# Kernel optimization log

Hardware: AMD Instinct MI355X
Metric: run time of the kernel (lower is better)

Reference implementation:

```python
import jax, jax.numpy as jnp
import numpy as np
from jax.ops import segment_sum

N_NODES = 100000
N_EDGES = 3200000
NUM_FEATURES = 256


def setup_inputs() -> dict:
    key = jax.random.key(0)
    ks = jax.random.split(key, 12)
    def lin(k, fan_in, fan_out):
        bound = 1.0 / np.sqrt(fan_in)
        kw, kb = jax.random.split(k)
        W = jax.random.uniform(kw, (fan_in, fan_out), jnp.float32, -bound, bound)
        b = jax.random.uniform(kb, (fan_out,), jnp.float32, -bound, bound)
        return W, b
    x = jax.random.normal(ks[0], (N_NODES, NUM_FEATURES), jnp.float32)
    edge_index = jax.random.randint(ks[1], (2, N_EDGES), 0, N_NODES, jnp.int64 if jax.config.jax_enable_x64 else jnp.int32)
    W1, b1 = lin(ks[2], NUM_FEATURES, 64)
    W2, b2 = lin(ks[3], 64, 32)
    W3, b3 = lin(ks[4], 32, 16)
    Ws02, bs02 = lin(ks[5], NUM_FEATURES, 32)
    Ws03, bs03 = lin(ks[6], NUM_FEATURES, 16)
    Ws13, bs13 = lin(ks[7], 64, 16)
    Wout, bout = lin(ks[8], 16, 1)
    return dict(x=x, edge_index=edge_index, W1=W1, b1=b1, W2=W2, b2=b2,
                W3=W3, b3=b3, Ws02=Ws02, bs02=bs02, Ws03=Ws03, bs03=bs03,
                Ws13=Ws13, bs13=bs13, Wout=Wout, bout=bout)


def _deg_inv_sqrt(edge_index, n_nodes):
    # gcn_norm with self-loops: degree counted at target nodes, +1 for self-loop
    dst = edge_index[1]
    deg = segment_sum(jnp.ones(edge_index.shape[1], jnp.float32), dst, num_segments=n_nodes) + 1.0
    return jnp.where(deg > 0, jax.lax.rsqrt(deg), 0.0)


def _gcn_conv(x, W, b, edge_index, dinv):
    # PyG GCNConv: h = x W; out[i] = sum_{j->i} dinv[j]*dinv[i]*h[j] + dinv[i]^2*h[i] + b
    src, dst = edge_index[0], edge_index[1]
    h = x @ W                                   # [N, out]
    norm = (dinv[src] * dinv[dst])[:, None]     # [E, 1]
    agg = segment_sum(h[src] * norm, dst, num_segments=x.shape[0])
    agg = agg + (dinv * dinv)[:, None] * h      # self-loop term
    return agg + b


def reference(x, edge_index, W1, b1, W2, b2, W3, b3,
              Ws02, bs02, Ws03, bs03, Ws13, bs13, Wout, bout):
    # Dropout in eval mode (identity).
    dinv = _deg_inv_sqrt(edge_index, x.shape[0])
    x1 = jax.nn.relu(_gcn_conv(x, W1, b1, edge_index, dinv))
    x2 = jax.nn.relu(_gcn_conv(x1, W2, b2, edge_index, dinv) + x @ Ws02 + bs02)
    x3 = jax.nn.relu(_gcn_conv(x2, W3, b3, edge_index, dinv)
                     + x @ Ws03 + bs03 + x1 @ Ws13 + bs13)
    return jax.nn.sigmoid(x3 @ Wout + bout)
```

## Files before the change

### kernel.cpp

```cpp
#include <hip/hip_runtime.h>
#include <hip/hip_bf16.h>
#include <math.h>


#define NBUCK_MAX 512
#define P1_CHUNK 4096
#define EPT 16
#define BCAP 9216
#define PREP_BLOCKS 142
#define HIST_BLOCKS 1024

typedef __attribute__((ext_vector_type(8))) short bfrag;
typedef __attribute__((ext_vector_type(4))) float f4_t;
typedef __attribute__((ext_vector_type(2))) float f2_t;

__device__ inline float uaf(unsigned u) { return __uint_as_float(u); }
__device__ inline ushort f2bf(float f) {
    __hip_bfloat16 b = __float2bfloat16(f);
    return *reinterpret_cast<ushort*>(&b);
}
__device__ inline unsigned scale2(unsigned w, float s) {
    const float lo = uaf(w << 16) * s;
    const float hi = uaf(w & 0xffff0000u) * s;
    return (unsigned)f2bf(lo) | ((unsigned)f2bf(hi) << 16);
}
__device__ inline bfrag cvt8(const float4 a, const float4 b) {
    union { ushort u[8]; bfrag f; } r;
    r.u[0] = f2bf(a.x); r.u[1] = f2bf(a.y); r.u[2] = f2bf(a.z); r.u[3] = f2bf(a.w);
    r.u[4] = f2bf(b.x); r.u[5] = f2bf(b.y); r.u[6] = f2bf(b.z); r.u[7] = f2bf(b.w);
    return r.f;
}
__device__ inline bfrag ld_bfrag(const ushort* p) {
    const uint4 raw = *reinterpret_cast<const uint4*>(p);
    return *reinterpret_cast<const bfrag*>(&raw);
}


__global__ __launch_bounds__(256) void fka_kernel(
    const float* __restrict__ W1, const float* __restrict__ Ws02,
    const float* __restrict__ Ws03, const float* __restrict__ W2,
    const float* __restrict__ Ws13, const float* __restrict__ W3,
    ushort* __restrict__ Wt0, ushort* __restrict__ Wt1, ushort* __restrict__ Wt2,
    const int* __restrict__ dst, int E, int* __restrict__ bucket_count,
    int nbuckets)
{
    if (blockIdx.x < PREP_BLOCKS) {
        const int idx = blockIdx.x * 256 + threadIdx.x;
        if (idx < 32768) {
            int f = idx >> 8, k = idx & 255;
            float v = 0.f;
            if (f < 64)       v = W1[k * 64 + f];
            else if (f < 96)  v = Ws02[k * 32 + (f - 64)];
            else if (f < 112) v = Ws03[k * 16 + (f - 96)];
            Wt0[idx] = f2bf(v);
        } else if (idx < 32768 + 3072) {
            int t = idx - 32768;
            int f = t >> 6, k = t & 63;
            float v = (f < 32) ? W2[k * 32 + f] : Ws13[k * 16 + (f - 32)];
            Wt1[t] = f2bf(v);
        } else if (idx < 32768 + 3072 + 512) {
            int t = idx - 32768 - 3072;
            int f = t >> 5, k = t & 31;
            Wt2[t] = f2bf(W3[k * 16 + f]);
        }
        return;
    }
    __shared__ int lhist[NBUCK_MAX];
    const int bid = blockIdx.x - PREP_BLOCKS;
    for (int i = threadIdx.x; i < nbuckets; i += 256) lhist[i] = 0;
    __syncthreads();
    const int stride = HIST_BLOCKS * 256;
    for (int e = bid * 256 + threadIdx.x; e < E; e += stride)
        atomicAdd(&lhist[dst[e] >> 8], 1);
    __syncthreads();
    for (int i = threadIdx.x; i < nbuckets; i += 256) {
        int c = lhist[i];
        if (c) atomicAdd(&bucket_count[i], c);
    }
}


__global__ __launch_bounds__(512) void bucket_scan_kernel(
    const int* __restrict__ bucket_count, int* __restrict__ bucket_base,
    int* __restrict__ bucket_cursor, int nbuckets)
{
    __shared__ int tmp[512];
    const int tid = threadIdx.x;
    int v = (tid < nbuckets) ? bucket_count[tid] : 0;
    tmp[tid] = v;
    __syncthreads();
    for (int off = 1; off < 512; off <<= 1) {
        int t = (tid >= off) ? tmp[tid - off] : 0;
        __syncthreads();
        tmp[tid] += t;
        __syncthreads();
    }
    if (tid < nbuckets) {
        int base = tmp[tid] - v;
        bucket_base[tid]   = base;
        bucket_cursor[tid] = base;
    }
}


union FKBsh {
    float xs[2][4096];
    struct {
        int hist[NBUCK_MAX];
        int lofs[NBUCK_MAX];
        int gbase[NBUCK_MAX];
        int lcur[NBUCK_MAX];
        int ssum[256];
        unsigned int stage[P1_CHUNK];
        int gidx[P1_CHUNK];
    } p;
};

__global__ __launch_bounds__(256, 3) void fkb_kernel(
    const int* __restrict__ src, const int* __restrict__ dst, int E,
    int* __restrict__ bucket_cursor, unsigned int* __restrict__ keys,
    int nbuckets, int part_blocks,
    const float* __restrict__ X, const ushort* __restrict__ Wt0,
    const float* __restrict__ bs02, const float* __restrict__ bs03,
    ushort* __restrict__ g1, float* __restrict__ pre2,
    float* __restrict__ pre3, int N)
{
    __shared__ __align__(16) FKBsh sh;
    const int tid = threadIdx.x;

    if (blockIdx.x < part_blocks) {
        const int e0 = blockIdx.x * P1_CHUNK;
        const int nE = min(P1_CHUNK, E - e0);

        for (int i = tid; i < NBUCK_MAX; i += 256) { sh.p.hist[i] = 0; sh.p.lcur[i] = 0; }
        __syncthreads();

        int myb[EPT];
        unsigned int mypk[EPT];
#pragma unroll
        for (int j = 0; j < EPT; ++j) {
            const int e = e0 + tid + j * 256;
            if (e < E) {
                const int d = dst[e];
                myb[j]  = d >> 8;
                mypk[j] = ((unsigned int)(d & 255) << 17) | (unsigned int)src[e];
                atomicAdd(&sh.p.hist[myb[j]], 1);
            } else myb[j] = -1;
        }
        __syncthreads();

        int a0 = (2 * tid     < nbuckets) ? sh.p.hist[2 * tid]     : 0;
        int a1 = (2 * tid + 1 < nbuckets) ? sh.p.hist[2 * tid + 1] : 0;
        sh.p.ssum[tid] = a0 + a1;
        __syncthreads();
        for (int off = 1; off < 256; off <<= 1) {
            int t = (tid >= off) ? sh.p.ssum[tid - off] : 0;
            __syncthreads();
            sh.p.ssum[tid] += t;
            __syncthreads();
        }
        const int ex = sh.p.ssum[tid] - (a0 + a1);
        if (2 * tid     < nbuckets) sh.p.lofs[2 * tid]     = ex;
        if (2 * tid + 1 < nbuckets) sh.p.lofs[2 * tid + 1] = ex + a0;
        __syncthreads();

        for (int i = tid; i < nbuckets; i += 256)
            sh.p.gbase[i] = atomicAdd(&bucket_cursor[i], sh.p.hist[i]);
        __syncthreads();

#pragma unroll
        for (int j = 0; j < EPT; ++j) {
            if (myb[j] >= 0) {
                const int b = myb[j];
                const int l = sh.p.lofs[b] + atomicAdd(&sh.p.lcur[b], 1);
                sh.p.stage[l] = mypk[j];
                sh.p.gidx[l]  = sh.p.gbase[b] - sh.p.lofs[b] + l;
            }
        }
        __syncthreads();

        for (int i = tid; i < nE; i += 256)
            keys[sh.p.gidx[i]] = sh.p.stage[i];
        return;
    }

    const int bid  = blockIdx.x - part_blocks;
    const int lane = tid & 63;
    const int wf   = tid >> 6;
    const int n0   = bid * 64;
    const int mrow = lane & 15;
    const int q    = lane >> 4;
    const int kq   = q * 8;

    bfrag bfr[2][8];
#pragma unroll
    for (int ft = 0; ft < 2; ++ft) {
        const ushort* wr = &Wt0[(size_t)(wf * 32 + ft * 16 + mrow) * 256 + kq];
#pragma unroll
        for (int p = 0; p < 8; ++p)
            bfr[ft][p] = ld_bfrag(&wr[p * 32]);
    }

    int srow[4], schunk[4];
#pragma unroll
    for (int j = 0; j < 4; ++j) {
        const int R = wf * 16 + j * 4 + q;
        srow[j]   = min(n0 + R, N - 1);
        schunk[j] = mrow ^ (R & 7);
    }

    auto STAGE = [&](int buf, int kc) {
#pragma unroll
        for (int j = 0; j < 4; ++j) {
            const float* gsrc =
                X + (size_t)srow[j] * 256 + kc * 64 + schunk[j] * 4;
            __builtin_amdgcn_global_load_lds(
                (const __attribute__((address_space(1))) unsigned int*)gsrc,
                (__attribute__((address_space(3))) unsigned int*)
                    &sh.xs[buf][(wf * 16 + j * 4) * 64],
                16, 0, 0);
        }
    };

    f4_t acc[4][2];
#pragma unroll
    for (int a = 0; a < 4; ++a)
#pragma unroll
        for (int b = 0; b < 2; ++b) acc[a][b] = {0.f, 0.f, 0.f, 0.f};

    STAGE(0, 0);
    __syncthreads();

    int cur = 0;
    for (int kc = 0; kc < 4; ++kc) {
        if (kc < 3) STAGE(cur ^ 1, kc + 1);
        const float4* Xs4 = reinterpret_cast<const float4*>(&sh.xs[cur][0]);
#pragma unroll
        for (int pl = 0; pl < 2; ++pl) {
            bfrag af[4];
#pragma unroll
            for (int mt = 0; mt < 4; ++mt) {
                const int r  = mt * 16 + mrow;
                const int c0 = pl * 8 + q * 2;
                const float4 u0 = Xs4[r * 16 + (c0 ^ (r & 7))];
                const float4 u1 = Xs4[r * 16 + ((c0 + 1) ^ (r & 7))];
                af[mt] = cvt8(u0, u1);
            }
            const int pg = kc * 2 + pl;
#pragma unroll
            for (int mt = 0; mt < 4; ++mt)
#pragma unroll
                for (int ft = 0; ft < 2; ++ft)
                    acc[mt][ft] = __builtin_amdgcn_mfma_f32_16x16x32_bf16(
                        af[mt], bfr[ft][pg], acc[mt][ft], 0, 0, 0);
        }
        __syncthreads();
        cur ^= 1;
    }

    char* sm = (char*)&sh;
    ushort* g1s = (ushort*)sm;
    float*  p2s = (float*)(sm + 8192);
    float*  p3s = (float*)(sm + 16384);

    if (wf < 2) {
#pragma unroll
        for (int mt = 0; mt < 4; ++mt) {
#pragma unroll
            for (int r = 0; r < 4; ++r) {
                const int nl = mt * 16 + q * 4 + r;
#pragma unroll
                for (int ft = 0; ft < 2; ++ft)
                    g1s[nl * 64 + wf * 32 + ft * 16 + mrow] =
                        f2bf(acc[mt][ft][r]);
            }
        }
    } else if (wf == 2) {
#pragma unroll
        for (int mt = 0; mt < 4; ++mt)
#pragma unroll
            for (int ft = 0; ft < 2; ++ft)
#pragma unroll
                for (int r = 0; r < 4; ++r)
                    p2s[(mt * 16 + q * 4 + r) * 32 + ft * 16 + mrow] =
                        acc[mt][ft][r] + bs02[ft * 16 + mrow];
    } else {
#pragma unroll
        for (int mt = 0; mt < 4; ++mt)
#pragma unroll
            for (int r = 0; r < 4; ++r)
                p3s[(mt * 16 + q * 4 + r) * 16 + mrow] =
                    acc[mt][0][r] + bs03[mrow];
    }
    __syncthreads();

    const uint4* g1v = (const uint4*)g1s;
    const uint4* p2v = (const uint4*)p2s;
    const uint4* p3v = (const uint4*)p3s;
#pragma unroll
    for (int t = 0; t < 2; ++t) {
        const int i   = t * 256 + tid;
        const int row = i >> 3;
        if (n0 + row < N)
            *(uint4*)(g1 + (size_t)(n0 + row) * 64 + (i & 7) * 8) = g1v[i];
    }
#pragma unroll
    for (int t = 0; t < 2; ++t) {
        const int i   = t * 256 + tid;
        const int row = i >> 3;
        if (n0 + row < N)
            *(uint4*)(pre2 + (size_t)(n0 + row) * 32 + (i & 7) * 4) = p2v[i];
    }
    {
        const int i   = tid;
        const int row = i >> 2;
        if (n0 + row < N)
            *(uint4*)(pre3 + (size_t)(n0 + row) * 16 + (i & 3) * 4) = p3v[i];
    }
}


__global__ __launch_bounds__(256) void csr_build_kernel(
    const unsigned int* __restrict__ keys, const int* __restrict__ bucket_base,
    const int* __restrict__ bucket_count,
    int* __restrict__ row_off, float* __restrict__ dinv, int* __restrict__ col,
    ushort* __restrict__ g1, int N, int E)
{
    __shared__ unsigned int inb[BCAP];
    __shared__ int outv[BCAP];
    __shared__ int hist[256];
    __shared__ int lofs[256];
    __shared__ int ssum[256];
    __shared__ float sdinv[256];

    const int tid  = threadIdx.x;
    const int b    = blockIdx.x;
    const int base = bucket_base[b];
    const int cnt  = min(bucket_count[b], BCAP);
    const int n0   = b << 8;
    const int nn   = min(256, N - n0);

    for (int i = tid; i < cnt; i += 256) inb[i] = keys[base + i];
    hist[tid] = 0;
    __syncthreads();

    for (int i = tid; i < cnt; i += 256)
        atomicAdd(&hist[inb[i] >> 17], 1);
    __syncthreads();

    ssum[tid] = hist[tid];
    __syncthreads();
    for (int off = 1; off < 256; off <<= 1) {
        int t = (tid >= off) ? ssum[tid - off] : 0;
        __syncthreads();
        ssum[tid] += t;
        __syncthreads();
    }
    lofs[tid] = ssum[tid] - hist[tid];

    if (tid < nn) {
        const float dv = rsqrtf((float)hist[tid] + 1.0f);
        row_off[n0 + tid] = base + lofs[tid];
        dinv[n0 + tid]    = dv;
        sdinv[tid]        = dv;
    }
    if (b == 0 && tid == 0) row_off[N] = E;
    __syncthreads();

    for (int i = tid; i < nn * 8; i += 256) {
        const int row = i >> 3, ch = i & 7;
        uint4* pp = reinterpret_cast<uint4*>(g1 + (size_t)(n0 + row) * 64 + ch * 8);
        const float dv = sdinv[row];
        uint4 v = *pp;
        v.x = scale2(v.x, dv); v.y = scale2(v.y, dv);
        v.z = scale2(v.z, dv); v.w = scale2(v.w, dv);
        *pp = v;
    }

    hist[tid] = 0;
    __syncthreads();

    for (int i = tid; i < cnt; i += 256) {
        const unsigned int k = inb[i];
        const int node = k >> 17;
        const int l = lofs[node] + atomicAdd(&hist[node], 1);
        outv[l] = (int)(k & 0x1FFFF);
    }
    __syncthreads();

    for (int i = tid; i < cnt; i += 256)
        col[base + i] = outv[i];
}


__global__ __launch_bounds__(256) void gemm_mfma1(
    const ushort* __restrict__ X1, const ushort* __restrict__ Wt1,
    const float* __restrict__ bs13, const float* __restrict__ dinv,
    __hip_bfloat16* __restrict__ g2, float* __restrict__ pre3, int N)
{
    __shared__ __align__(16) ushort g2s[128 * 32];
    __shared__ __align__(16) float  p3s[128 * 16];

    const int tid  = threadIdx.x;
    const int lane = tid & 63;
    const int wave = tid >> 6;
    const int nb   = blockIdx.x * 128;
    const int n0   = nb + wave * 32;
    const int mrow = lane & 15;
    const int q    = lane >> 4;
    const int kq   = q * 8;

    f4_t acc[2][3];
#pragma unroll
    for (int a = 0; a < 2; ++a)
#pragma unroll
        for (int b = 0; b < 3; ++b) acc[a][b] = {0.f, 0.f, 0.f, 0.f};

    const ushort* xrow[2];
#pragma unroll
    for (int mt = 0; mt < 2; ++mt) {
        int r = n0 + mt * 16 + mrow;
        r = (r < N) ? r : (N - 1);
        xrow[mt] = &X1[(size_t)r * 64 + kq];
    }
    const ushort* wrow[3];
#pragma unroll
    for (int ft = 0; ft < 3; ++ft)
        wrow[ft] = &Wt1[(size_t)(ft * 16 + mrow) * 64 + kq];

#pragma unroll
    for (int p = 0; p < 2; ++p) {
        bfrag af[2], bf[3];
#pragma unroll
        for (int mt = 0; mt < 2; ++mt) af[mt] = ld_bfrag(&xrow[mt][p * 32]);
#pragma unroll
        for (int ft = 0; ft < 3; ++ft) bf[ft] = ld_bfrag(&wrow[ft][p * 32]);
#pragma unroll
        for (int mt = 0; mt < 2; ++mt)
#pragma unroll
            for (int ft = 0; ft < 3; ++ft)
                acc[mt][ft] = __builtin_amdgcn_mfma_f32_16x16x32_bf16(
                    af[mt], bf[ft], acc[mt][ft], 0, 0, 0);
    }

#pragma unroll
    for (int mt = 0; mt < 2; ++mt) {
#pragma unroll
        for (int r = 0; r < 4; ++r) {
            const int nl = wave * 32 + mt * 16 + q * 4 + r;
            const float di = dinv[min(nb + nl, N - 1)];
            g2s[nl * 32 +      mrow] = f2bf(di * acc[mt][0][r]);
            g2s[nl * 32 + 16 + mrow] = f2bf(di * acc[mt][1][r]);
            p3s[nl * 16 + mrow] = acc[mt][2][r] + bs13[mrow];
        }
    }
    __syncthreads();

    const uint4*  g2v = (const uint4*)g2s;
    const float4* p3v = (const float4*)p3s;
#pragma unroll
    for (int t = 0; t < 2; ++t) {
        const int i   = t * 256 + tid;
        const int row = i >> 2;
        if (nb + row < N)
            *(uint4*)((ushort*)g2 + (size_t)(nb + row) * 32 + (i & 3) * 8) =
                g2v[i];
    }
#pragma unroll
    for (int t = 0; t < 2; ++t) {
        const int i   = t * 256 + tid;
        const int row = i >> 2;
        if (nb + row < N) {
            float4* dst =
                (float4*)(pre3 + (size_t)(nb + row) * 16 + (i & 3) * 4);
            float4 v = *dst;
            const float4 s = p3v[i];
            v.x += s.x; v.y += s.y; v.z += s.z; v.w += s.w;
            *dst = v;
        }
    }
}


template<int F, int MODE>
__global__ __launch_bounds__(256) void agg_kernel(
    const ushort* __restrict__ g, const float* __restrict__ dinv,
    const int* __restrict__ row_off, const int* __restrict__ col,
    const float* __restrict__ bias, const float* __restrict__ pre,
    const ushort* __restrict__ Wk,
    const float* __restrict__ Wout, const float* __restrict__ bout,
    void* __restrict__ out, int N)
{
    constexpr int FG  = F / 8;
    constexpr int EPW = 64 / FG;
    constexpr int U   = 32 / EPW;
    constexpr int LSH = (F == 64) ? 7 : (F == 32 ? 6 : 5);

    const int lane = threadIdx.x & 63;
    const int wv   = threadIdx.x >> 6;
    const int i    = blockIdx.x * 4 + wv;
    if (i >= N) return;

    const int fg  = lane & (FG - 1);
    const int eo  = lane / FG;
    const unsigned fbb = (unsigned)fg * 16;

    const char* gb = (const char*)g;

    f2_t acc0 = {0.f, 0.f}, acc1 = {0.f, 0.f};
    f2_t acc2 = {0.f, 0.f}, acc3 = {0.f, 0.f};

    const int s = row_off[i], e = row_off[i + 1];
    const int nfull = (e - s) >> 5;
    int p = s;
    const int* cp = col + s + eo;

    for (int it = 0; it < nfull; ++it, p += 32, cp += 32) {
        unsigned voff[U];
#pragma unroll
        for (int u = 0; u < U; ++u)
            voff[u] = ((unsigned)cp[u * EPW] << LSH) + fbb;
        uint4 w[U];
#pragma unroll
        for (int u = 0; u < U; ++u)
            w[u] = *reinterpret_cast<const uint4*>(gb + voff[u]);
#pragma unroll
        for (int u = 0; u < U; ++u) {
            acc0 += (f2_t){uaf(w[u].x << 16), uaf(w[u].x & 0xffff0000u)};
            acc1 += (f2_t){uaf(w[u].y << 16), uaf(w[u].y & 0xffff0000u)};
            acc2 += (f2_t){uaf(w[u].z << 16), uaf(w[u].z & 0xffff0000u)};
            acc3 += (f2_t){uaf(w[u].w << 16), uaf(w[u].w & 0xffff0000u)};
        }
    }
    if (p < e) {
        float m[U];
        unsigned voff[U];
#pragma unroll
        for (int u = 0; u < U; ++u) {
            const int q = p + eo + u * EPW;
            m[u]    = (q < e) ? 1.0f : 0.0f;
            voff[u] = ((unsigned)col[min(q, e - 1)] << LSH) + fbb;
        }
        uint4 w[U];
#pragma unroll
        for (int u = 0; u < U; ++u)
            w[u] = *reinterpret_cast<const uint4*>(gb + voff[u]);
#pragma unroll
        for (int u = 0; u < U; ++u) {
            const f2_t mm = {m[u], m[u]};
            acc0 += mm * (f2_t){uaf(w[u].x << 16), uaf(w[u].x & 0xffff0000u)};
            acc1 += mm * (f2_t){uaf(w[u].y << 16), uaf(w[u].y & 0xffff0000u)};
            acc2 += mm * (f2_t){uaf(w[u].z << 16), uaf(w[u].z & 0xffff0000u)};
            acc3 += mm * (f2_t){uaf(w[u].w << 16), uaf(w[u].w & 0xffff0000u)};
        }
    }

#pragma unroll
    for (int ro = FG; ro < 64; ro <<= 1) {
        acc0.x += __shfl_xor(acc0.x, ro); acc0.y += __shfl_xor(acc0.y, ro);
        acc1.x += __shfl_xor(acc1.x, ro); acc1.y += __shfl_xor(acc1.y, ro);
        acc2.x += __shfl_xor(acc2.x, ro); acc2.y += __shfl_xor(acc2.y, ro);
        acc3.x += __shfl_xor(acc3.x, ro); acc3.y += __shfl_xor(acc3.y, ro);
    }

    const uint4 ws =
        *reinterpret_cast<const uint4*>(gb + (((unsigned)i) << LSH) + fbb);
    const float di = dinv[i];
    const int fb = fg * 8;
    const float4 b0 = *reinterpret_cast<const float4*>(&bias[fb]);
    const float4 b1 = *reinterpret_cast<const float4*>(&bias[fb + 4]);

    float v0 = di * (acc0.x + uaf(ws.x << 16))         + b0.x;
    float v1 = di * (acc0.y + uaf(ws.x & 0xffff0000u)) + b0.y;
    float v2 = di * (acc1.x + uaf(ws.y << 16))         + b0.z;
    float v3 = di * (acc1.y + uaf(ws.y & 0xffff0000u)) + b0.w;
    float v4 = di * (acc2.x + uaf(ws.z << 16))         + b1.x;
    float v5 = di * (acc2.y + uaf(ws.z & 0xffff0000u)) + b1.y;
    float v6 = di * (acc3.x + uaf(ws.w << 16))         + b1.z;
    float v7 = di * (acc3.y + uaf(ws.w & 0xffff0000u)) + b1.w;

    if (MODE != 0) {
        const float4 p0 = *reinterpret_cast<const float4*>(&pre[(size_t)i * F + fb]);
        const float4 p1 = *reinterpret_cast<const float4*>(&pre[(size_t)i * F + fb + 4]);
        v0 += p0.x; v1 += p0.y; v2 += p0.z; v3 += p0.w;
        v4 += p1.x; v5 += p1.y; v6 += p1.z; v7 += p1.w;
    }
    v0 = fmaxf(v0, 0.f); v1 = fmaxf(v1, 0.f);
    v2 = fmaxf(v2, 0.f); v3 = fmaxf(v3, 0.f);
    v4 = fmaxf(v4, 0.f); v5 = fmaxf(v5, 0.f);
    v6 = fmaxf(v6, 0.f); v7 = fmaxf(v7, 0.f);

    if (MODE == 0) {
        if (lane < FG) {
            uint4 o;
            o.x = (unsigned)f2bf(v0) | ((unsigned)f2bf(v1) << 16);
            o.y = (unsigned)f2bf(v2) | ((unsigned)f2bf(v3) << 16);
            o.z = (unsigned)f2bf(v4) | ((unsigned)f2bf(v5) << 16);
            o.w = (unsigned)f2bf(v6) | ((unsigned)f2bf(v7) << 16);
            *reinterpret_cast<uint4*>((char*)out + (((size_t)i) << LSH) + fbb) = o;
        }
    } else if (MODE == 1) {
        const uint4 wr = *reinterpret_cast<const uint4*>(&Wk[eo * 32 + fb]);
        float sacc;
        sacc  = v0 * uaf(wr.x << 16);
        sacc += v1 * uaf(wr.x & 0xffff0000u);
        sacc += v2 * uaf(wr.y << 16);
        sacc += v3 * uaf(wr.y & 0xffff0000u);
        sacc += v4 * uaf(wr.z << 16);
        sacc += v5 * uaf(wr.z & 0xffff0000u);
        sacc += v6 * uaf(wr.w << 16);
        sacc += v7 * uaf(wr.w & 0xffff0000u);
        sacc += __shfl_xor(sacc, 1);
        sacc += __shfl_xor(sacc, 2);
        if ((lane & 3) == 0)
            ((ushort*)out)[(size_t)i * 16 + eo] = f2bf(di * sacc);
    } else {
        const float4 w0 = *reinterpret_cast<const float4*>(&Wout[fb]);
        const float4 w1 = *reinterpret_cast<const float4*>(&Wout[fb + 4]);
        float t = v0 * w0.x + v1 * w0.y + v2 * w0.z + v3 * w0.w +
                  v4 * w1.x + v5 * w1.y + v6 * w1.z + v7 * w1.w;
        t += __shfl_xor(t, 1);
        if (lane == 0)
            ((float*)out)[i] = 1.0f / (1.0f + expf(-(t + bout[0])));
    }
}


extern "C" void kernel_launch(void* const* d_in, const int* in_sizes, int n_in,
                              void* d_out, int out_size, void* d_ws, size_t ws_size,
                              hipStream_t stream)
{
    const float* x    = (const float*)d_in[0];
    const int*   edge = (const int*)d_in[1];
    const float* W1   = (const float*)d_in[2];
    const float* b1   = (const float*)d_in[3];
    const float* W2   = (const float*)d_in[4];
    const float* b2   = (const float*)d_in[5];
    const float* W3   = (const float*)d_in[6];
    const float* b3   = (const float*)d_in[7];
    const float* Ws02 = (const float*)d_in[8];
    const float* bs02 = (const float*)d_in[9];
    const float* Ws03 = (const float*)d_in[10];
    const float* bs03 = (const float*)d_in[11];
    const float* Ws13 = (const float*)d_in[12];
    const float* bs13 = (const float*)d_in[13];
    const float* Wout = (const float*)d_in[14];
    const float* bout = (const float*)d_in[15];

    const int N = in_sizes[0] / 256;
    const int E = in_sizes[1] / 2;
    const int* srcv = edge;
    const int* dstv = edge + E;
    const int nbuckets = (N + 255) >> 8;

    char* ws = (char*)d_ws;
    size_t off = 0;
    auto alloc = [&](size_t bytes) -> void* {
        void* p = ws + off;
        off += (bytes + 255) & ~(size_t)255;
        return p;
    };
    unsigned int* keys = (unsigned int*)alloc((size_t)E * 4);
    int*   col      = (int*)  alloc((size_t)E * 4);
    int*   bcount   = (int*)  alloc((size_t)NBUCK_MAX * 4);
    int*   bbase    = (int*)  alloc((size_t)NBUCK_MAX * 4);
    int*   bcursor  = (int*)  alloc((size_t)NBUCK_MAX * 4);
    int*   row_off  = (int*)  alloc((size_t)(N + 1) * 4);
    float* dinv     = (float*)alloc((size_t)N * 4);
    ushort* Wt0     = (ushort*)alloc((size_t)128 * 256 * 2);
    ushort* Wt1     = (ushort*)alloc((size_t)48 * 64 * 2);
    ushort* Wt2     = (ushort*)alloc((size_t)16 * 32 * 2);
    ushort* g1      = (ushort*)alloc((size_t)N * 64 * 2);
    ushort* x1      = (ushort*)alloc((size_t)N * 64 * 2);
    ushort* g2      = (ushort*)alloc((size_t)N * 32 * 2);
    ushort* g3      = (ushort*)alloc((size_t)N * 16 * 2);
    float* pre2     = (float*)alloc((size_t)N * 32 * 4);
    float* pre3     = (float*)alloc((size_t)N * 16 * 4);

    hipMemsetAsync(bcount, 0, (size_t)NBUCK_MAX * 4, stream);

    fka_kernel<<<PREP_BLOCKS + HIST_BLOCKS, 256, 0, stream>>>(
        W1, Ws02, Ws03, W2, Ws13, W3, Wt0, Wt1, Wt2,
        dstv, E, bcount, nbuckets);

    bucket_scan_kernel<<<1, 512, 0, stream>>>(bcount, bbase, bcursor, nbuckets);

    const int PB = (E + P1_CHUNK - 1) / P1_CHUNK;
    fkb_kernel<<<PB + (N + 63) / 64, 256, 0, stream>>>(
        srcv, dstv, E, bcursor, keys, nbuckets, PB,
        x, Wt0, bs02, bs03, g1, pre2, pre3, N);

    csr_build_kernel<<<nbuckets, 256, 0, stream>>>(
        keys, bbase, bcount, row_off, dinv, col, g1, N, E);

    const int ab = (N + 3) / 4;

    agg_kernel<64, 0><<<ab, 256, 0, stream>>>(
        g1, dinv, row_off, col, b1, nullptr, nullptr,
        nullptr, nullptr, x1, N);
    gemm_mfma1<<<(N + 127) / 128, 256, 0, stream>>>(
        x1, Wt1, bs13, dinv, (__hip_bfloat16*)g2, pre3, N);
    agg_kernel<32, 1><<<ab, 256, 0, stream>>>(
        g2, dinv, row_off, col, b2, pre2, Wt2,
        nullptr, nullptr, g3, N);
    agg_kernel<16, 2><<<ab, 256, 0, stream>>>(
        g3, dinv, row_off, col, b3, pre3, nullptr,
        Wout, bout, d_out, N);
}
```

Measured before the change: 426.5 us.

## Split partition from layer-0 GEMM and fold dinv scaling into GEMM epilogue

Separates the fused partition+GEMM kernel into a standalone partition kernel (with doubled chunk size and edges per thread) and a GEMM kernel launched after CSR build. The GEMM now applies the per-node dinv scaling in its epilogue before bf16 conversion, so the CSR build no longer rereads and rewrites g1. This removes a read-modify-write pass over g1 but gives up the concurrency of running partition and GEMM blocks in one launch, and the larger chunk raises register and shared-memory use in the partition kernel.

```diff
diff --git a/kernel.cpp b/kernel.cpp
--- a/kernel.cpp
+++ b/kernel.cpp
@@ -4,8 +4,8 @@
 
 
 #define NBUCK_MAX 512
-#define P1_CHUNK 4096
-#define EPT 16
+#define P1_CHUNK 8192
+#define EPT 32
 #define BCAP 9216
 #define PREP_BLOCKS 142
 #define HIST_BLOCKS 1024
@@ -18,11 +18,6 @@
 __device__ inline ushort f2bf(float f) {
     __hip_bfloat16 b = __float2bfloat16(f);
     return *reinterpret_cast<ushort*>(&b);
-}
-__device__ inline unsigned scale2(unsigned w, float s) {
-    const float lo = uaf(w << 16) * s;
-    const float hi = uaf(w & 0xffff0000u) * s;
-    return (unsigned)f2bf(lo) | ((unsigned)f2bf(hi) << 16);
 }
 __device__ inline bfrag cvt8(const float4 a, const float4 b) {
     union { ushort u[8]; bfrag f; } r;
@@ -103,91 +98,147 @@
 }
 
 
-union FKBsh {
-    float xs[2][4096];
-    struct {
-        int hist[NBUCK_MAX];
-        int lofs[NBUCK_MAX];
-        int gbase[NBUCK_MAX];
-        int lcur[NBUCK_MAX];
-        int ssum[256];
-        unsigned int stage[P1_CHUNK];
-        int gidx[P1_CHUNK];
-    } p;
-};
-
-__global__ __launch_bounds__(256, 3) void fkb_kernel(
+__global__ __launch_bounds__(256) void partition_kernel(
     const int* __restrict__ src, const int* __restrict__ dst, int E,
-    int* __restrict__ bucket_cursor, unsigned int* __restrict__ keys,
-    int nbuckets, int part_blocks,
+    int* __restrict__ bucket_cursor, unsigned int* __restrict__ keys, int nbuckets)
+{
+    __shared__ int hist[NBUCK_MAX];
+    __shared__ int lofs[NBUCK_MAX];
+    __shared__ int gbase[NBUCK_MAX];
+    __shared__ int lcur[NBUCK_MAX];
+    __shared__ int ssum[256];
+    __shared__ unsigned int stage[P1_CHUNK];
+    __shared__ int gidx[P1_CHUNK];
+
+    const int tid = threadIdx.x;
+    const int e0  = blockIdx.x * P1_CHUNK;
+    const int nE  = min(P1_CHUNK, E - e0);
+
+    for (int i = tid; i < NBUCK_MAX; i += 256) { hist[i] = 0; lcur[i] = 0; }
+    __syncthreads();
+
+    int myb[EPT];
+    unsigned int mypk[EPT];
+#pragma unroll
+    for (int j = 0; j < EPT; ++j) {
+        const int e = e0 + tid + j * 256;
+        if (e < E) {
+            const int d = dst[e];
+            myb[j]  = d >> 8;
+            mypk[j] = ((unsigned int)(d & 255) << 17) | (unsigned int)src[e];
+            atomicAdd(&hist[myb[j]], 1);
+        } else myb[j] = -1;
+    }
+    __syncthreads();
+
+    int a0 = (2 * tid     < nbuckets) ? hist[2 * tid]     : 0;
+    int a1 = (2 * tid + 1 < nbuckets) ? hist[2 * tid + 1] : 0;
+    ssum[tid] = a0 + a1;
+    __syncthreads();
+    for (int off = 1; off < 256; off <<= 1) {
+        int t = (tid >= off) ? ssum[tid - off] : 0;
+        __syncthreads();
+        ssum[tid] += t;
+        __syncthreads();
+    }
+    const int ex = ssum[tid] - (a0 + a1);
+    if (2 * tid     < nbuckets) lofs[2 * tid]     = ex;
+    if (2 * tid + 1 < nbuckets) lofs[2 * tid + 1] = ex + a0;
+    __syncthreads();
+
+    for (int i = tid; i < nbuckets; i += 256)
+        gbase[i] = atomicAdd(&bucket_cursor[i], hist[i]);
+    __syncthreads();
+
+#pragma unroll
+    for (int j = 0; j < EPT; ++j) {
+        if (myb[j] >= 0) {
+            const int b = myb[j];
+            const int l = lofs[b] + atomicAdd(&lcur[b], 1);
+            stage[l] = mypk[j];
+            gidx[l]  = gbase[b] - lofs[b] + l;
+        }
+    }
+    __syncthreads();
+
+    for (int i = tid; i < nE; i += 256)
+        keys[gidx[i]] = stage[i];
+}
+
+
+__global__ __launch_bounds__(256) void csr_build_kernel(
+    const unsigned int* __restrict__ keys, const int* __restrict__ bucket_base,
+    const int* __restrict__ bucket_count,
+    int* __restrict__ row_off, float* __restrict__ dinv, int* __restrict__ col,
+    int N, int E)
+{
+    __shared__ unsigned int inb[BCAP];
+    __shared__ int outv[BCAP];
+    __shared__ int hist[256];
+    __shared__ int lofs[256];
+    __shared__ int ssum[256];
+
+    const int tid  = threadIdx.x;
+    const int b    = blockIdx.x;
+    const int base = bucket_base[b];
+    const int cnt  = min(bucket_count[b], BCAP);
+    const int n0   = b << 8;
+    const int nn   = min(256, N - n0);
+
+    for (int i = tid; i < cnt; i += 256) inb[i] = keys[base + i];
+    hist[tid] = 0;
+    __syncthreads();
+
+    for (int i = tid; i < cnt; i += 256)
+        atomicAdd(&hist[inb[i] >> 17], 1);
+    __syncthreads();
+
+    ssum[tid] = hist[tid];
+    __syncthreads();
+    for (int off = 1; off < 256; off <<= 1) {
+        int t = (tid >= off) ? ssum[tid - off] : 0;
+        __syncthreads();
+        ssum[tid] += t;
+        __syncthreads();
+    }
+    lofs[tid] = ssum[tid] - hist[tid];
+
+    if (tid < nn) {
+        row_off[n0 + tid] = base + lofs[tid];
+        dinv[n0 + tid]    = rsqrtf((float)hist[tid] + 1.0f);
+    }
+    if (b == 0 && tid == 0) row_off[N] = E;
+    __syncthreads();
+
+    hist[tid] = 0;
+    __syncthreads();
+
+    for (int i = tid; i < cnt; i += 256) {
+        const unsigned int k = inb[i];
+        const int node = k >> 17;
+        const int l = lofs[node] + atomicAdd(&hist[node], 1);
+        outv[l] = (int)(k & 0x1FFFF);
+    }
+    __syncthreads();
+
+    for (int i = tid; i < cnt; i += 256)
+        col[base + i] = outv[i];
+}
+
+
+__global__ __launch_bounds__(256, 3) void gemm_mfma0(
     const float* __restrict__ X, const ushort* __restrict__ Wt0,
     const float* __restrict__ bs02, const float* __restrict__ bs03,
+    const float* __restrict__ dinv,
     ushort* __restrict__ g1, float* __restrict__ pre2,
     float* __restrict__ pre3, int N)
 {
-    __shared__ __align__(16) FKBsh sh;
-    const int tid = threadIdx.x;
-
-    if (blockIdx.x < part_blocks) {
-        const int e0 = blockIdx.x * P1_CHUNK;
-        const int nE = min(P1_CHUNK, E - e0);
-
-        for (int i = tid; i < NBUCK_MAX; i += 256) { sh.p.hist[i] = 0; sh.p.lcur[i] = 0; }
-        __syncthreads();
-
-        int myb[EPT];
-        unsigned int mypk[EPT];
-#pragma unroll
-        for (int j = 0; j < EPT; ++j) {
-            const int e = e0 + tid + j * 256;
-            if (e < E) {
-                const int d = dst[e];
-                myb[j]  = d >> 8;
-                mypk[j] = ((unsigned int)(d & 255) << 17) | (unsigned int)src[e];
-                atomicAdd(&sh.p.hist[myb[j]], 1);
-            } else myb[j] = -1;
-        }
-        __syncthreads();
-
-        int a0 = (2 * tid     < nbuckets) ? sh.p.hist[2 * tid]     : 0;
-        int a1 = (2 * tid + 1 < nbuckets) ? sh.p.hist[2 * tid + 1] : 0;
-        sh.p.ssum[tid] = a0 + a1;
-        __syncthreads();
-        for (int off = 1; off < 256; off <<= 1) {
-            int t = (tid >= off) ? sh.p.ssum[tid - off] : 0;
-            __syncthreads();
-            sh.p.ssum[tid] += t;
-            __syncthreads();
-        }
-        const int ex = sh.p.ssum[tid] - (a0 + a1);
-        if (2 * tid     < nbuckets) sh.p.lofs[2 * tid]     = ex;
-        if (2 * tid + 1 < nbuckets) sh.p.lofs[2 * tid + 1] = ex + a0;
-        __syncthreads();
-
-        for (int i = tid; i < nbuckets; i += 256)
-            sh.p.gbase[i] = atomicAdd(&bucket_cursor[i], sh.p.hist[i]);
-        __syncthreads();
-
-#pragma unroll
-        for (int j = 0; j < EPT; ++j) {
-            if (myb[j] >= 0) {
-                const int b = myb[j];
-                const int l = sh.p.lofs[b] + atomicAdd(&sh.p.lcur[b], 1);
-                sh.p.stage[l] = mypk[j];
-                sh.p.gidx[l]  = sh.p.gbase[b] - sh.p.lofs[b] + l;
-            }
-        }
-        __syncthreads();
-
-        for (int i = tid; i < nE; i += 256)
-            keys[sh.p.gidx[i]] = sh.p.stage[i];
-        return;
-    }
-
-    const int bid  = blockIdx.x - part_blocks;
+    __shared__ __align__(16) float Xs[2][64 * 64];
+
+    const int tid  = threadIdx.x;
     const int lane = tid & 63;
     const int wf   = tid >> 6;
-    const int n0   = bid * 64;
+    const int n0   = blockIdx.x * 64;
     const int mrow = lane & 15;
     const int q    = lane >> 4;
     const int kq   = q * 8;
@@ -217,7 +268,7 @@
             __builtin_amdgcn_global_load_lds(
                 (const __attribute__((address_space(1))) unsigned int*)gsrc,
                 (__attribute__((address_space(3))) unsigned int*)
-                    &sh.xs[buf][(wf * 16 + j * 4) * 64],
+                    &Xs[buf][(wf * 16 + j * 4) * 64],
                 16, 0, 0);
         }
     };
@@ -234,7 +285,7 @@
     int cur = 0;
     for (int kc = 0; kc < 4; ++kc) {
         if (kc < 3) STAGE(cur ^ 1, kc + 1);
-        const float4* Xs4 = reinterpret_cast<const float4*>(&sh.xs[cur][0]);
+        const float4* Xs4 = reinterpret_cast<const float4*>(&Xs[cur][0]);
 #pragma unroll
         for (int pl = 0; pl < 2; ++pl) {
             bfrag af[4];
@@ -258,7 +309,7 @@
         cur ^= 1;
     }
 
-    char* sm = (char*)&sh;
+    char* sm = (char*)Xs;
     ushort* g1s = (ushort*)sm;
     float*  p2s = (float*)(sm + 8192);
     float*  p3s = (float*)(sm + 16384);
@@ -269,10 +320,11 @@
 #pragma unroll
             for (int r = 0; r < 4; ++r) {
                 const int nl = mt * 16 + q * 4 + r;
+                const float di = dinv[min(n0 + nl, N - 1)];
 #pragma unroll
                 for (int ft = 0; ft < 2; ++ft)
                     g1s[nl * 64 + wf * 32 + ft * 16 + mrow] =
-                        f2bf(acc[mt][ft][r]);
+                        f2bf(di * acc[mt][ft][r]);
             }
         }
     } else if (wf == 2) {
@@ -317,79 +369,6 @@
         if (n0 + row < N)
             *(uint4*)(pre3 + (size_t)(n0 + row) * 16 + (i & 3) * 4) = p3v[i];
     }
-}
-
-
-__global__ __launch_bounds__(256) void csr_build_kernel(
-    const unsigned int* __restrict__ keys, const int* __restrict__ bucket_base,
-    const int* __restrict__ bucket_count,
-    int* __restrict__ row_off, float* __restrict__ dinv, int* __restrict__ col,
-    ushort* __restrict__ g1, int N, int E)
-{
-    __shared__ unsigned int inb[BCAP];
-    __shared__ int outv[BCAP];
-    __shared__ int hist[256];
-    __shared__ int lofs[256];
-    __shared__ int ssum[256];
-    __shared__ float sdinv[256];
-
-    const int tid  = threadIdx.x;
-    const int b    = blockIdx.x;
-    const int base = bucket_base[b];
-    const int cnt  = min(bucket_count[b], BCAP);
-    const int n0   = b << 8;
-    const int nn   = min(256, N - n0);
-
-    for (int i = tid; i < cnt; i += 256) inb[i] = keys[base + i];
-    hist[tid] = 0;
-    __syncthreads();
-
-    for (int i = tid; i < cnt; i += 256)
-        atomicAdd(&hist[inb[i] >> 17], 1);
-    __syncthreads();
-
-    ssum[tid] = hist[tid];
-    __syncthreads();
-    for (int off = 1; off < 256; off <<= 1) {
-        int t = (tid >= off) ? ssum[tid - off] : 0;
-        __syncthreads();
-        ssum[tid] += t;
-        __syncthreads();
-    }
-    lofs[tid] = ssum[tid] - hist[tid];
-
-    if (tid < nn) {
-        const float dv = rsqrtf((float)hist[tid] + 1.0f);
-        row_off[n0 + tid] = base + lofs[tid];
-        dinv[n0 + tid]    = dv;
-        sdinv[tid]        = dv;
-    }
-    if (b == 0 && tid == 0) row_off[N] = E;
-    __syncthreads();
-
-    for (int i = tid; i < nn * 8; i += 256) {
-        const int row = i >> 3, ch = i & 7;
-        uint4* pp = reinterpret_cast<uint4*>(g1 + (size_t)(n0 + row) * 64 + ch * 8);
-        const float dv = sdinv[row];
-        uint4 v = *pp;
-        v.x = scale2(v.x, dv); v.y = scale2(v.y, dv);
-        v.z = scale2(v.z, dv); v.w = scale2(v.w, dv);
-        *pp = v;
-    }
-
-    hist[tid] = 0;
-    __syncthreads();
-
-    for (int i = tid; i < cnt; i += 256) {
-        const unsigned int k = inb[i];
-        const int node = k >> 17;
-        const int l = lofs[node] + atomicAdd(&hist[node], 1);
-        outv[l] = (int)(k & 0x1FFFF);
-    }
-    __syncthreads();
-
-    for (int i = tid; i < cnt; i += 256)
-        col[base + i] = outv[i];
 }
 
 
@@ -685,13 +664,14 @@
 
     bucket_scan_kernel<<<1, 512, 0, stream>>>(bcount, bbase, bcursor, nbuckets);
 
-    const int PB = (E + P1_CHUNK - 1) / P1_CHUNK;
-    fkb_kernel<<<PB + (N + 63) / 64, 256, 0, stream>>>(
-        srcv, dstv, E, bcursor, keys, nbuckets, PB,
-        x, Wt0, bs02, bs03, g1, pre2, pre3, N);
+    partition_kernel<<<(E + P1_CHUNK - 1) / P1_CHUNK, 256, 0, stream>>>(
+        srcv, dstv, E, bcursor, keys, nbuckets);
 
     csr_build_kernel<<<nbuckets, 256, 0, stream>>>(
-        keys, bbase, bcount, row_off, dinv, col, g1, N, E);
+        keys, bbase, bcount, row_off, dinv, col, N, E);
+
+    gemm_mfma0<<<(N + 63) / 64, 256, 0, stream>>>(
+        x, Wt0, bs02, bs03, dinv, g1, pre2, pre3, N);
 
     const int ab = (N + 3) / 4;
 
```

Measured after the change: 419.7 us. Within noise of the previous version (-1.6%).
